# Optimization experiments

Hardware: AMD Instinct MI355X
Metric: run time of the kernel (lower is better)

Reference implementation:

```python
import jax, jax.numpy as jnp
import numpy as np

THRESHOLD = 20.0
CIRCLE_OFFSETS = [(0, -3), (1, -3), (2, -2), (3, -1), (3, 0), (3, 1), (2, 2), (1, 3),
                  (0, 3), (-1, 3), (-2, 2), (-3, 1), (-3, 0), (-3, -1), (-2, -2), (-1, -3)]


def setup_inputs() -> dict:
    key = jax.random.key(0)
    image = jax.random.uniform(key, (4, 1, 1080, 1920), dtype=jnp.float32) * 255.0
    return {"image": image}


def _detect_9_consecutive(bits_16):
    # bits_16: int32 (N, H, W). Build 24-bit circular buffer, test all 16 rotations
    # for 9 consecutive set bits (window == 511) using arithmetic-only ops.
    lower_8 = bits_16 % 256
    buffer_24 = bits_16 + lower_8 * 65536  # (N, H, W) int32
    divisors = (jnp.int32(2) ** jnp.arange(16, dtype=jnp.int32)).reshape(16, 1, 1, 1)
    shifted = (buffer_24[None] // divisors) % 512  # (16, N, H, W)
    return jnp.any(shifted == 511, axis=0)  # (N, H, W) bool


def reference(image):
    N, C, H, W = image.shape
    img = image.astype(jnp.float32)
    # Replicate-pad by 3 and gather the 16 Bresenham circle pixels via shifted slices.
    padded = jnp.pad(img[:, 0], ((0, 0), (3, 3), (3, 3)), mode='edge')  # (N, H+6, W+6)
    circle = jnp.stack(
        [padded[:, 3 + dy:3 + dy + H, 3 + dx:3 + dx + W] for dy, dx in CIRCLE_OFFSETS],
        axis=-1)  # (N, H, W, 16)
    center = img[:, 0][..., None]  # (N, H, W, 1)
    diff = circle - center
    powers = (jnp.int32(1) << jnp.arange(16, dtype=jnp.int32)).reshape(1, 1, 1, 16)
    dark_bits = ((diff >= THRESHOLD).astype(jnp.int32) * powers).sum(axis=-1)
    bright_bits = ((diff <= -THRESHOLD).astype(jnp.int32) * powers).sum(axis=-1)
    detected = _detect_9_consecutive(dark_bits) | _detect_9_consecutive(bright_bits)
    return detected.astype(jnp.float32)[:, None]  # (N, 1, H, W)
```

## Files before the change

### kernel.cpp

```cpp
#include <hip/hip_runtime.h>

#define IMG_H 1080
#define IMG_W 1920

__device__ __forceinline__ unsigned det9(unsigned m) {
    unsigned x = m | (m << 16);
    unsigned t = x & (x >> 1);
    t &= t >> 2;
    t &= t >> 4;
    t &= x >> 8;
    return t;
}

#define STEP_GE(m, sc, val, thr)                                          \
    asm("v_cmp_ge_f32 %1, %2, %3\n\tv_addc_co_u32 %0, %1, %0, %0, %1"     \
        : "+v"(m), "=s"(sc) : "v"(val), "v"(thr))
#define STEP_LE(m, sc, val, thr)                                          \
    asm("v_cmp_le_f32 %1, %2, %3\n\tv_addc_co_u32 %0, %1, %0, %0, %1"     \
        : "+v"(m), "=s"(sc) : "v"(val), "v"(thr))

__global__ __launch_bounds__(256) void fast_score_kernel(const float* __restrict__ img,
                                                         float* __restrict__ out) {
    const int n  = blockIdx.z;
    const int y  = blockIdx.y;
    const int gx = blockIdx.x * 256 + threadIdx.x;

    const float* base = img + (size_t)n * (IMG_H * IMG_W);

    const float* rp[7];
#pragma unroll
    for (int d = 0; d < 7; ++d) {
        const int ry = min(max(y + d - 3, 0), IMG_H - 1);
        rp[d] = base + (size_t)ry * IMG_W;
    }

    int c[7];
#pragma unroll
    for (int d = 0; d < 7; ++d) {
        c[d] = min(max(gx + d - 3, 0), IMG_W - 1);
    }

    constexpr int DY[16] = {0, 1, 2, 3, 3, 3, 2, 1, 0, -1, -2, -3, -3, -3, -2, -1};
    constexpr int DX[16] = {-3, -3, -2, -1, 0, 1, 2, 3, 3, 3, 2, 1, 0, -1, -2, -3};

    const float center = rp[3][c[3]];
    float t[16];
#pragma unroll
    for (int k = 0; k < 16; ++k) {
        t[k] = rp[DY[k] + 3][c[DX[k] + 3]];
    }

    const float hi = center + 20.0f;
    const float lo = center - 20.0f;
    unsigned dark = 0u, bright = 0u;
    unsigned long long sc0, sc1;
#pragma unroll
    for (int k = 0; k < 16; ++k) {
        STEP_GE(dark,   sc0, t[k], hi);
        STEP_LE(bright, sc1, t[k], lo);
    }

    const float res = (det9(dark) | det9(bright)) ? 1.0f : 0.0f;
    if (gx < IMG_W) {
        out[(size_t)n * (IMG_H * IMG_W) + (size_t)y * IMG_W + gx] = res;
    }
}

extern "C" void kernel_launch(void* const* d_in, const int* in_sizes, int n_in,
                              void* d_out, int out_size, void* d_ws, size_t ws_size,
                              hipStream_t stream) {
    const float* img = (const float*)d_in[0];
    float* out = (float*)d_out;
    const int n_img = in_sizes[0] / (IMG_H * IMG_W);
    dim3 grid((IMG_W + 255) / 256,
              IMG_H,
              n_img);
    fast_score_kernel<<<grid, 256, 0, stream>>>(img, out);
}
```

Before: 98.65 us.

## Compute eight pixels per thread with float4 row loads and XCD block remap

Each thread now loads a 7x16 float window with vectorized float4 loads and evaluates the FAST test for 8 adjacent pixels, storing results as two float4 writes. Blocks become 32x8 tiles with a 1D grid remapped round-robin across XCDs. This replaces 17 scalar loads per pixel with shared register reuse, cutting load instruction count and address arithmetic. The cost is higher register pressure and a scalar clamped fallback path at the image edges.

```diff
diff --git a/kernel.cpp b/kernel.cpp
--- a/kernel.cpp
+++ b/kernel.cpp
@@ -2,6 +2,10 @@
 
 #define IMG_H 1080
 #define IMG_W 1920
+#define TILE_W 256
+#define TILE_H 8
+#define GXB ((IMG_W + TILE_W - 1) / TILE_W)
+#define GYB (IMG_H / TILE_H)
 
 __device__ __forceinline__ unsigned det9(unsigned m) {
     unsigned x = m | (m << 16);
@@ -19,11 +23,30 @@
     asm("v_cmp_le_f32 %1, %2, %3\n\tv_addc_co_u32 %0, %1, %0, %0, %1"     \
         : "+v"(m), "=s"(sc) : "v"(val), "v"(thr))
 
+__device__ __forceinline__ float f4_get(const float4& v, int c) {
+    return c == 0 ? v.x : c == 1 ? v.y : c == 2 ? v.z : v.w;
+}
+__device__ __forceinline__ void f4_set(float4& v, int c, float x) {
+    if (c == 0) v.x = x; else if (c == 1) v.y = x; else if (c == 2) v.z = x; else v.w = x;
+}
+
 __global__ __launch_bounds__(256) void fast_score_kernel(const float* __restrict__ img,
                                                          float* __restrict__ out) {
-    const int n  = blockIdx.z;
-    const int y  = blockIdx.y;
-    const int gx = blockIdx.x * 256 + threadIdx.x;
+    int bid = blockIdx.x;
+    const int nwg = gridDim.x;
+    if ((nwg & 7) == 0) {
+        bid = (bid & 7) * (nwg >> 3) + (bid >> 3);
+    }
+    const int bx  = bid % GXB;
+    const int byz = bid / GXB;
+    const int by  = byz % GYB;
+    const int n   = byz / GYB;
+
+    const int tx = threadIdx.x;
+    const int ty = threadIdx.y;
+
+    const int gx0 = bx * TILE_W + tx * 8;
+    const int y   = by * TILE_H + ty;
 
     const float* base = img + (size_t)n * (IMG_H * IMG_W);
 
@@ -34,35 +57,53 @@
         rp[d] = base + (size_t)ry * IMG_W;
     }
 
-    int c[7];
+    const int c0 = gx0 - 4;
+    float4 r[7][4];
+    if (c0 >= 0 && c0 + 16 <= IMG_W) {
 #pragma unroll
-    for (int d = 0; d < 7; ++d) {
-        c[d] = min(max(gx + d - 3, 0), IMG_W - 1);
+        for (int d = 0; d < 7; ++d) {
+            const float4* p = (const float4*)(rp[d] + c0);
+            r[d][0] = p[0];
+            r[d][1] = p[1];
+            r[d][2] = p[2];
+            r[d][3] = p[3];
+        }
+    } else {
+#pragma unroll
+        for (int d = 0; d < 7; ++d) {
+#pragma unroll
+            for (int j = 0; j < 16; ++j) {
+                const int cc = min(max(c0 + j, 0), IMG_W - 1);
+                f4_set(r[d][j >> 2], j & 3, rp[d][cc]);
+            }
+        }
     }
 
     constexpr int DY[16] = {0, 1, 2, 3, 3, 3, 2, 1, 0, -1, -2, -3, -3, -3, -2, -1};
     constexpr int DX[16] = {-3, -3, -2, -1, 0, 1, 2, 3, 3, 3, 2, 1, 0, -1, -2, -3};
 
-    const float center = rp[3][c[3]];
-    float t[16];
+    float res[8];
 #pragma unroll
-    for (int k = 0; k < 16; ++k) {
-        t[k] = rp[DY[k] + 3][c[DX[k] + 3]];
+    for (int i = 0; i < 8; ++i) {
+        const float center = f4_get(r[3][(i + 4) >> 2], (i + 4) & 3);
+        const float hi = center + 20.0f;
+        const float lo = center - 20.0f;
+        unsigned dark = 0u, bright = 0u;
+        unsigned long long sc0, sc1;
+#pragma unroll
+        for (int k = 0; k < 16; ++k) {
+            const int w = i + DX[k] + 4;
+            const float t = f4_get(r[DY[k] + 3][w >> 2], w & 3);
+            STEP_GE(dark,   sc0, t, hi);
+            STEP_LE(bright, sc1, t, lo);
+        }
+        res[i] = (det9(dark) | det9(bright)) ? 1.0f : 0.0f;
     }
 
-    const float hi = center + 20.0f;
-    const float lo = center - 20.0f;
-    unsigned dark = 0u, bright = 0u;
-    unsigned long long sc0, sc1;
-#pragma unroll
-    for (int k = 0; k < 16; ++k) {
-        STEP_GE(dark,   sc0, t[k], hi);
-        STEP_LE(bright, sc1, t[k], lo);
-    }
-
-    const float res = (det9(dark) | det9(bright)) ? 1.0f : 0.0f;
-    if (gx < IMG_W) {
-        out[(size_t)n * (IMG_H * IMG_W) + (size_t)y * IMG_W + gx] = res;
+    if (gx0 < IMG_W) {
+        float* o = out + (size_t)n * (IMG_H * IMG_W) + (size_t)y * IMG_W + gx0;
+        *(float4*)(o)     = make_float4(res[0], res[1], res[2], res[3]);
+        *(float4*)(o + 4) = make_float4(res[4], res[5], res[6], res[7]);
     }
 }
 
@@ -72,8 +113,7 @@
     const float* img = (const float*)d_in[0];
     float* out = (float*)d_out;
     const int n_img = in_sizes[0] / (IMG_H * IMG_W);
-    dim3 grid((IMG_W + 255) / 256,
-              IMG_H,
-              n_img);
-    fast_score_kernel<<<grid, 256, 0, stream>>>(img, out);
+    dim3 grid(GXB * GYB * n_img, 1, 1);
+    dim3 block(32, 8, 1);
+    fast_score_kernel<<<grid, block, 0, stream>>>(img, out);
 }
```

New measurement: 234.5 us. +137.8%, slower.

## Stage haloed 128x8 image tiles in LDS and remap blocks across XCDs

Applied to the files above, without the earlier changes.

Each block now loads a 14x136 haloed band of the image into shared memory with float4 loads (clamped scalar loads at the image edges). Each thread then computes four output rows by reading the 16 circle pixels from LDS instead of global memory. The 1D grid is remapped so neighbouring tiles go to the same XCD for L2 locality. This trades many redundant global gathers for one cooperative load, at the cost of a barrier and LDS pressure.

```diff
diff --git a/kernel.cpp b/kernel.cpp
--- a/kernel.cpp
+++ b/kernel.cpp
@@ -2,6 +2,13 @@
 
 #define IMG_H 1080
 #define IMG_W 1920
+#define TILE_W 128
+#define TILE_H 8
+#define GXB (IMG_W / TILE_W)
+#define GYB (IMG_H / TILE_H)
+#define BAND_H (TILE_H + 6)
+#define BAND_W 136
+#define BAND_W4 (BAND_W / 4)
 
 __device__ __forceinline__ unsigned det9(unsigned m) {
     unsigned x = m | (m << 16);
@@ -21,48 +28,80 @@
 
 __global__ __launch_bounds__(256) void fast_score_kernel(const float* __restrict__ img,
                                                          float* __restrict__ out) {
-    const int n  = blockIdx.z;
-    const int y  = blockIdx.y;
-    const int gx = blockIdx.x * 256 + threadIdx.x;
+    __shared__ float band[BAND_H][BAND_W];
+
+    int bid = blockIdx.x;
+    {
+        const int nwg = gridDim.x;
+        const int q = nwg >> 3, r = nwg & 7;
+        const int xcd = bid & 7, idx = bid >> 3;
+        bid = (xcd < r ? xcd * (q + 1) : r * (q + 1) + (xcd - r) * q) + idx;
+    }
+    const int bx = bid % GXB;
+    const int t0 = bid / GXB;
+    const int by = t0 % GYB;
+    const int n  = t0 / GYB;
+
+    const int tx  = threadIdx.x;
+    const int ty  = threadIdx.y;
+    const int tid = ty * TILE_W + tx;
+
+    const int gx0 = bx * TILE_W;
+    const int y0  = by * TILE_H;
 
     const float* base = img + (size_t)n * (IMG_H * IMG_W);
 
-    const float* rp[7];
+    if (bx > 0 && bx < GXB - 1) {
 #pragma unroll
-    for (int d = 0; d < 7; ++d) {
-        const int ry = min(max(y + d - 3, 0), IMG_H - 1);
-        rp[d] = base + (size_t)ry * IMG_W;
+        for (int i = tid; i < BAND_H * BAND_W4; i += 256) {
+            const int r = i / BAND_W4;
+            const int c = i - r * BAND_W4;
+            const int ry = min(max(y0 - 3 + r, 0), IMG_H - 1);
+            const float4 v =
+                *(const float4*)(base + (size_t)ry * IMG_W + (gx0 - 4 + c * 4));
+            *(float4*)&band[r][c * 4] = v;
+        }
+    } else {
+        for (int i = tid; i < BAND_H * BAND_W; i += 256) {
+            const int r  = i / BAND_W;
+            const int c  = i - r * BAND_W;
+            const int ry = min(max(y0 - 3 + r, 0), IMG_H - 1);
+            const int cx = min(max(gx0 - 4 + c, 0), IMG_W - 1);
+            band[r][c] = base[(size_t)ry * IMG_W + cx];
+        }
     }
-
-    int c[7];
-#pragma unroll
-    for (int d = 0; d < 7; ++d) {
-        c[d] = min(max(gx + d - 3, 0), IMG_W - 1);
-    }
+    __syncthreads();
 
     constexpr int DY[16] = {0, 1, 2, 3, 3, 3, 2, 1, 0, -1, -2, -3, -3, -3, -2, -1};
     constexpr int DX[16] = {-3, -3, -2, -1, 0, 1, 2, 3, 3, 3, 2, 1, 0, -1, -2, -3};
 
-    const float center = rp[3][c[3]];
-    float t[16];
+    const int cx = tx + 4;
+    float* obase = out + (size_t)n * (IMG_H * IMG_W) + (size_t)y0 * IMG_W + gx0 + tx;
+
 #pragma unroll
-    for (int k = 0; k < 16; ++k) {
-        t[k] = rp[DY[k] + 3][c[DX[k] + 3]];
-    }
+    for (int i = 0; i < 4; ++i) {
+        const int j  = ty * 4 + i;
+        const int rr = j + 3;
 
-    const float hi = center + 20.0f;
-    const float lo = center - 20.0f;
-    unsigned dark = 0u, bright = 0u;
-    unsigned long long sc0, sc1;
+        const float center = band[rr][cx];
+        const float hi = center + 20.0f;
+        const float lo = center - 20.0f;
+
+        float tv[16];
 #pragma unroll
-    for (int k = 0; k < 16; ++k) {
-        STEP_GE(dark,   sc0, t[k], hi);
-        STEP_LE(bright, sc1, t[k], lo);
-    }
+        for (int k = 0; k < 16; ++k) {
+            tv[k] = band[rr + DY[k]][cx + DX[k]];
+        }
 
-    const float res = (det9(dark) | det9(bright)) ? 1.0f : 0.0f;
-    if (gx < IMG_W) {
-        out[(size_t)n * (IMG_H * IMG_W) + (size_t)y * IMG_W + gx] = res;
+        unsigned dark = 0u, bright = 0u;
+        unsigned long long sc0, sc1;
+#pragma unroll
+        for (int k = 0; k < 16; ++k) {
+            STEP_GE(dark,   sc0, tv[k], hi);
+            STEP_LE(bright, sc1, tv[k], lo);
+        }
+
+        obase[(size_t)j * IMG_W] = (det9(dark) | det9(bright)) ? 1.0f : 0.0f;
     }
 }
 
@@ -72,8 +111,7 @@
     const float* img = (const float*)d_in[0];
     float* out = (float*)d_out;
     const int n_img = in_sizes[0] / (IMG_H * IMG_W);
-    dim3 grid((IMG_W + 255) / 256,
-              IMG_H,
-              n_img);
-    fast_score_kernel<<<grid, 256, 0, stream>>>(img, out);
+    dim3 grid(GXB * GYB * n_img, 1, 1);
+    dim3 block(TILE_W, 2, 1);
+    fast_score_kernel<<<grid, block, 0, stream>>>(img, out);
 }
```

New measurement: 97.04 us. No clear change (-1.6%).
